# Kernel tuning notes

Measured on AMD Instinct MI355X. Metric: run time of the kernel, lower is better.

## Reference

```python
import jax, jax.numpy as jnp
import numpy as np

N_NODES = 40000


def gcn_conv(x, edge_index, W, b, num_nodes):
    """PyG GCNConv: add self-loops, sym-normalize, x @ W.T then scatter-add, + bias."""
    src = edge_index[0]
    dst = edge_index[1]
    loop = jnp.arange(num_nodes, dtype=src.dtype)
    src = jnp.concatenate([src, loop])
    dst = jnp.concatenate([dst, loop])
    # linear transform first (PyG applies lin before propagate)
    h = x @ W.T  # [N, out]
    # symmetric normalization: deg over destination (with self-loops)
    deg = jax.ops.segment_sum(jnp.ones_like(dst, dtype=h.dtype), dst, num_segments=num_nodes)
    dinv = jnp.where(deg > 0, jax.lax.rsqrt(deg), 0.0)
    norm = dinv[src] * dinv[dst]  # [E+N]
    msg = h[src] * norm[:, None]  # gather + scale
    out = jax.ops.segment_sum(msg, dst, num_segments=num_nodes)  # scatter-add
    return out + b


def setup_inputs() -> dict:
    key = jax.random.key(0)
    k1, k2, k3, k4, k5, k6, k7 = jax.random.split(key, 7)
    C, H, F_out = 128, 128, 1
    E = 640000
    x = jax.random.normal(k1, (N_NODES, C), dtype=jnp.float32)
    edge_index = jax.random.randint(k2, (2, E), 0, N_NODES, dtype=jnp.int64)
    # Glorot-ish init for conv weights (PyG lin.weight shape [out, in]), zero bias
    W1 = jax.random.normal(k3, (H, C), dtype=jnp.float32) / np.sqrt(C)
    b1 = jnp.zeros((H,), dtype=jnp.float32)
    W2 = jax.random.normal(k4, (F_out, H), dtype=jnp.float32) / np.sqrt(H)
    b2 = jnp.zeros((F_out,), dtype=jnp.float32)
    return {"x": x, "edge_index": edge_index, "W1": W1, "b1": b1, "W2": W2, "b2": b2}


def reference(x, edge_index, W1, b1, W2, b2):
    h = gcn_conv(x, edge_index, W1, b1, N_NODES)
    h = jax.nn.relu(h)
    out = gcn_conv(h, edge_index, W2, b2, N_NODES)
    return jax.nn.sigmoid(out)
```

## Files before the change

### kernel.cpp

```cpp
#include <hip/hip_runtime.h>
#include <math.h>
#include <stdint.h>

#define FDIM 128
#define CAP 64

typedef __bf16 bf16x8 __attribute__((ext_vector_type(8)));
typedef float f32x4 __attribute__((ext_vector_type(4)));

__device__ __forceinline__ ushort f2bf(float f) {
    uint32_t u = __float_as_uint(f);
    uint32_t r = (u >> 16) & 1;
    return (ushort)((u + 0x7fffu + r) >> 16);
}


#define XS 136

__global__ __launch_bounds__(256) void k_linear1_mfma(const float* __restrict__ x,
                                                      const float* __restrict__ W,
                                                      int* __restrict__ cnt,
                                                      ushort* __restrict__ h, int n) {
    __shared__ __align__(16) ushort Wl[128 * XS];
    __shared__ __align__(16) ushort Xl[64 * XS];

    int tid = threadIdx.x;

    if (tid < 128) {
        int g = blockIdx.x * 128 + tid;
        if (g < n) cnt[g] = 0;
    }

#pragma unroll
    for (int i = 0; i < 16; ++i) {
        int q = tid + i * 256;
        int j = q >> 5;
        int c0 = (q & 31) * 4;
        float4 v = *(const float4*)(W + (size_t)q * 4);
        uint2 p;
        p.x = (uint32_t)f2bf(v.x) | ((uint32_t)f2bf(v.y) << 16);
        p.y = (uint32_t)f2bf(v.z) | ((uint32_t)f2bf(v.w) << 16);
        *(uint2*)&Wl[j * XS + c0] = p;
    }

    int lane = tid & 63, wid = tid >> 6;
    int m0 = (wid >> 1) * 32;
    int j0 = (wid & 1) * 64;
    int lrow = lane & 15, kg = lane >> 4;

    for (int t = 0; t < 2; ++t) {
        int node0 = blockIdx.x * 128 + t * 64;
        if (node0 >= n) break;

        __syncthreads();
#pragma unroll
        for (int i = 0; i < 8; ++i) {
            int q = tid + i * 256;
            int r = q >> 5;
            int c0 = (q & 31) * 4;
            int gr = node0 + r;
            float4 v = make_float4(0.f, 0.f, 0.f, 0.f);
            if (gr < n) v = *(const float4*)(x + (size_t)gr * FDIM + c0);
            uint2 p;
            p.x = (uint32_t)f2bf(v.x) | ((uint32_t)f2bf(v.y) << 16);
            p.y = (uint32_t)f2bf(v.z) | ((uint32_t)f2bf(v.w) << 16);
            *(uint2*)&Xl[r * XS + c0] = p;
        }
        __syncthreads();

        bf16x8 af[2][4];
#pragma unroll
        for (int mt = 0; mt < 2; ++mt)
#pragma unroll
            for (int ks = 0; ks < 4; ++ks)
                af[mt][ks] = *(const bf16x8*)&Xl[(m0 + mt * 16 + lrow) * XS + ks * 32 + kg * 8];

        f32x4 acc[2][4] = {};
#pragma unroll
        for (int jt = 0; jt < 4; ++jt) {
            bf16x8 bfr[4];
#pragma unroll
            for (int ks = 0; ks < 4; ++ks)
                bfr[ks] = *(const bf16x8*)&Wl[(j0 + jt * 16 + lrow) * XS + ks * 32 + kg * 8];
#pragma unroll
            for (int mt = 0; mt < 2; ++mt)
#pragma unroll
                for (int ks = 0; ks < 4; ++ks)
                    acc[mt][jt] = __builtin_amdgcn_mfma_f32_16x16x32_bf16(
                        af[mt][ks], bfr[ks], acc[mt][jt], 0, 0, 0);
        }

#pragma unroll
        for (int mt = 0; mt < 2; ++mt)
#pragma unroll
            for (int jt = 0; jt < 4; ++jt)
#pragma unroll
                for (int r = 0; r < 4; ++r) {
                    int gi = node0 + m0 + mt * 16 + kg * 4 + r;
                    int gj = j0 + jt * 16 + lrow;
                    if (gi < n) h[(size_t)gi * FDIM + gj] = f2bf(acc[mt][jt][r]);
                }
    }
}


__global__ __launch_bounds__(256) void k_scatter_ell(const int* __restrict__ src,
                                                     const int* __restrict__ dst,
                                                     int* __restrict__ cnt,
                                                     ushort* __restrict__ ell, int E) {
    int e = blockIdx.x * blockDim.x + threadIdx.x;
    if (e < E) {
        int d = dst[e];
        int p = atomicAdd(&cnt[d], 1);
        if (p < CAP) ell[(size_t)d * CAP + p] = (ushort)src[e];
    }
}


__device__ __forceinline__ float bf_lo(uint32_t u) { return __uint_as_float(u << 16); }
__device__ __forceinline__ float bf_hi(uint32_t u) { return __uint_as_float(u & 0xFFFF0000u); }

__global__ __launch_bounds__(256) void k_agg1_h2(const uint32_t* __restrict__ h,
                                                 const ushort* __restrict__ ell,
                                                 const int* __restrict__ cnt,
                                                 const float* __restrict__ b1,
                                                 const float* __restrict__ W2,
                                                 float* __restrict__ h2s, int n) {
    int gtid = blockIdx.x * blockDim.x + threadIdx.x;
    int d = gtid >> 6;
    int lane = threadIdx.x & 63;
    if (d >= n) return;

    int degt = cnt[d];
    int deg = min(degt, CAP);
    int myidx = 0;
    float mydv = 0.f;
    if (lane < deg) {
        myidx = (int)ell[(size_t)d * CAP + lane];
        mydv = rsqrtf((float)cnt[myidx] + 1.0f);
    }

    float dd = rsqrtf((float)degt + 1.0f);
    uint32_t u = h[(size_t)d * 64 + lane];
    float ax[8], ay[8];
    ax[0] = bf_lo(u) * dd; ay[0] = bf_hi(u) * dd;
#pragma unroll
    for (int r = 1; r < 8; ++r) { ax[r] = 0.f; ay[r] = 0.f; }

    int k = 0;
    for (; k + 7 < deg; k += 8) {
        int s[8]; float dv[8]; uint32_t uu[8];
#pragma unroll
        for (int r = 0; r < 8; ++r) { s[r] = __shfl(myidx, k + r); dv[r] = __shfl(mydv, k + r); }
#pragma unroll
        for (int r = 0; r < 8; ++r) uu[r] = h[(size_t)s[r] * 64 + lane];
#pragma unroll
        for (int r = 0; r < 8; ++r) { ax[r] += bf_lo(uu[r]) * dv[r]; ay[r] += bf_hi(uu[r]) * dv[r]; }
    }
    for (; k + 3 < deg; k += 4) {
        int s[4]; float dv[4]; uint32_t uu[4];
#pragma unroll
        for (int r = 0; r < 4; ++r) { s[r] = __shfl(myidx, k + r); dv[r] = __shfl(mydv, k + r); }
#pragma unroll
        for (int r = 0; r < 4; ++r) uu[r] = h[(size_t)s[r] * 64 + lane];
#pragma unroll
        for (int r = 0; r < 4; ++r) { ax[r] += bf_lo(uu[r]) * dv[r]; ay[r] += bf_hi(uu[r]) * dv[r]; }
    }
    for (; k < deg; ++k) {
        int s0 = __shfl(myidx, k);
        float dv0 = __shfl(mydv, k);
        uint32_t u0 = h[(size_t)s0 * 64 + lane];
        ax[0] += bf_lo(u0) * dv0; ay[0] += bf_hi(u0) * dv0;
    }

    float sx = ((ax[0] + ax[1]) + (ax[2] + ax[3])) + ((ax[4] + ax[5]) + (ax[6] + ax[7]));
    float sy = ((ay[0] + ay[1]) + (ay[2] + ay[3])) + ((ay[4] + ay[5]) + (ay[6] + ay[7]));

    float ox = sx * dd;
    float oy = sy * dd;

    float2 bb = *(const float2*)(b1 + lane * 2);
    float2 ww = *(const float2*)(W2 + lane * 2);
    float s = fmaxf(ox + bb.x, 0.f) * ww.x + fmaxf(oy + bb.y, 0.f) * ww.y;
#pragma unroll
    for (int o = 32; o; o >>= 1) s += __shfl_down(s, o);
    if (lane == 0) h2s[d] = s * dd;
}


__global__ __launch_bounds__(256) void k_agg2(const float* __restrict__ h2s,
                                              const ushort* __restrict__ ell,
                                              const int* __restrict__ cnt,
                                              const float* __restrict__ b2,
                                              float* __restrict__ out, int n) {
    int gtid = blockIdx.x * blockDim.x + threadIdx.x;
    int i = gtid >> 6;
    int lane = threadIdx.x & 63;
    if (i >= n) return;

    int degt = cnt[i];
    int deg = min(degt, CAP);
    float v = 0.f;
    if (lane < deg) {
        int s = ell[(size_t)i * CAP + lane];
        v = h2s[s];
    }
#pragma unroll
    for (int o = 32; o; o >>= 1) v += __shfl_down(v, o);
    if (lane == 0) {
        float dd = rsqrtf((float)degt + 1.0f);
        float r = (h2s[i] + v) * dd + b2[0];
        out[i] = 1.f / (1.f + expf(-r));
    }
}


extern "C" void kernel_launch(void* const* d_in, const int* in_sizes, int n_in,
                              void* d_out, int out_size, void* d_ws, size_t ws_size,
                              hipStream_t stream) {
    const float* x  = (const float*)d_in[0];
    const int*   ei = (const int*)d_in[1];
    const float* W1 = (const float*)d_in[2];
    const float* b1 = (const float*)d_in[3];
    const float* W2 = (const float*)d_in[4];
    const float* b2 = (const float*)d_in[5];

    int n = out_size;
    int E = in_sizes[1] / 2;
    const int* src = ei;
    const int* dst = ei + E;

    char* w = (char*)d_ws;
    int*    cnt = (int*)w;     w += (size_t)((n + 3) & ~3) * 4;
    ushort* ell = (ushort*)w;  w += (size_t)n * CAP * 2;
    ushort* h1s = (ushort*)w;  w += (size_t)n * FDIM * 2;
    float*  h2s = (float*)w;   w += (size_t)n * 4;

    int nblk_lin = (n + 127) / 128;

    k_linear1_mfma<<<nblk_lin, 256, 0, stream>>>(x, W1, cnt, h1s, n);
    k_scatter_ell<<<(E + 255) / 256, 256, 0, stream>>>(src, dst, cnt, ell, E);
    k_agg1_h2<<<(n * 64 + 255) / 256, 256, 0, stream>>>((const uint32_t*)h1s, ell, cnt, b1, W2, h2s, n);
    k_agg2<<<(n * 64 + 255) / 256, 256, 0, stream>>>(h2s, ell, cnt, b2, (float*)d_out, n);
}
```

Baseline: 85.58 us.

## Merge linear and edge-scatter kernels, pre-convert W1 to bf16 in prep kernel

Adds a small prep kernel that converts W1 to padded bf16 once and zeroes the degree counters with int4 stores. The linear MFMA kernel and the ELL scatter kernel become one launch, with block ranges split by role, so the atomic scatter can overlap the GEMM. Each linear block now covers 256 nodes instead of 128, which amortises the W tile copy into LDS. The scatter blocks still allocate the large LDS footprint, which may limit how many run at once, and an extra launch is added.

```diff
diff --git a/kernel.cpp b/kernel.cpp
--- a/kernel.cpp
+++ b/kernel.cpp
@@ -4,6 +4,7 @@
 
 #define FDIM 128
 #define CAP 64
+#define XS 136
 
 typedef __bf16 bf16x8 __attribute__((ext_vector_type(8)));
 typedef float f32x4 __attribute__((ext_vector_type(4)));
@@ -15,32 +16,52 @@
 }
 
 
-#define XS 136
-
-__global__ __launch_bounds__(256) void k_linear1_mfma(const float* __restrict__ x,
-                                                      const float* __restrict__ W,
-                                                      int* __restrict__ cnt,
-                                                      ushort* __restrict__ h, int n) {
-    __shared__ __align__(16) ushort Wl[128 * XS];
-    __shared__ __align__(16) ushort Xl[64 * XS];
-
-    int tid = threadIdx.x;
-
-    if (tid < 128) {
-        int g = blockIdx.x * 128 + tid;
-        if (g < n) cnt[g] = 0;
-    }
-
-#pragma unroll
-    for (int i = 0; i < 16; ++i) {
-        int q = tid + i * 256;
-        int j = q >> 5;
-        int c0 = (q & 31) * 4;
-        float4 v = *(const float4*)(W + (size_t)q * 4);
+__global__ __launch_bounds__(256) void k_prep(const float* __restrict__ W,
+                                              ushort* __restrict__ Wb,
+                                              int4* __restrict__ cnt4, int n4) {
+    int t = blockIdx.x * blockDim.x + threadIdx.x;
+    if (t < 4096) {
+        float4 v = *(const float4*)(W + (size_t)t * 4);
+        int j = t >> 5, c0 = (t & 31) * 4;
         uint2 p;
         p.x = (uint32_t)f2bf(v.x) | ((uint32_t)f2bf(v.y) << 16);
         p.y = (uint32_t)f2bf(v.z) | ((uint32_t)f2bf(v.w) << 16);
-        *(uint2*)&Wl[j * XS + c0] = p;
+        *(uint2*)&Wb[j * XS + c0] = p;
+    } else {
+        int z = t - 4096;
+        if (z < n4) cnt4[z] = make_int4(0, 0, 0, 0);
+    }
+}
+
+
+__global__ __launch_bounds__(256) void k_lin_scatter(const float* __restrict__ x,
+                                                     const ushort* __restrict__ Wb,
+                                                     const int* __restrict__ src,
+                                                     const int* __restrict__ dst,
+                                                     int* __restrict__ cnt,
+                                                     ushort* __restrict__ ell,
+                                                     ushort* __restrict__ h,
+                                                     int n, int E) {
+    int NL = (n + 255) >> 8;
+    int tid = threadIdx.x;
+
+    if ((int)blockIdx.x >= NL) {
+        int e = ((int)blockIdx.x - NL) * 256 + tid;
+        if (e < E) {
+            int d = dst[e];
+            int p = atomicAdd(&cnt[d], 1);
+            if (p < CAP) ell[(size_t)d * CAP + p] = (ushort)src[e];
+        }
+        return;
+    }
+
+    __shared__ __align__(16) ushort Wl[128 * XS];
+    __shared__ __align__(16) ushort Xl[64 * XS];
+
+    {
+        const uint4* wsrc = (const uint4*)Wb;
+        uint4* wdst = (uint4*)Wl;
+        for (int i = tid; i < (128 * XS) / 8; i += 256) wdst[i] = wsrc[i];
     }
 
     int lane = tid & 63, wid = tid >> 6;
@@ -48,8 +69,8 @@
     int j0 = (wid & 1) * 64;
     int lrow = lane & 15, kg = lane >> 4;
 
-    for (int t = 0; t < 2; ++t) {
-        int node0 = blockIdx.x * 128 + t * 64;
+    for (int t = 0; t < 4; ++t) {
+        int node0 = (int)blockIdx.x * 256 + t * 64;
         if (node0 >= n) break;
 
         __syncthreads();
@@ -104,19 +125,6 @@
 }
 
 
-__global__ __launch_bounds__(256) void k_scatter_ell(const int* __restrict__ src,
-                                                     const int* __restrict__ dst,
-                                                     int* __restrict__ cnt,
-                                                     ushort* __restrict__ ell, int E) {
-    int e = blockIdx.x * blockDim.x + threadIdx.x;
-    if (e < E) {
-        int d = dst[e];
-        int p = atomicAdd(&cnt[d], 1);
-        if (p < CAP) ell[(size_t)d * CAP + p] = (ushort)src[e];
-    }
-}
-
-
 __device__ __forceinline__ float bf_lo(uint32_t u) { return __uint_as_float(u << 16); }
 __device__ __forceinline__ float bf_hi(uint32_t u) { return __uint_as_float(u & 0xFFFF0000u); }
 
@@ -232,14 +240,18 @@
 
     char* w = (char*)d_ws;
     int*    cnt = (int*)w;     w += (size_t)((n + 3) & ~3) * 4;
+    ushort* Wb  = (ushort*)w;  w += (size_t)128 * XS * 2;
     ushort* ell = (ushort*)w;  w += (size_t)n * CAP * 2;
     ushort* h1s = (ushort*)w;  w += (size_t)n * FDIM * 2;
     float*  h2s = (float*)w;   w += (size_t)n * 4;
 
-    int nblk_lin = (n + 127) / 128;
-
-    k_linear1_mfma<<<nblk_lin, 256, 0, stream>>>(x, W1, cnt, h1s, n);
-    k_scatter_ell<<<(E + 255) / 256, 256, 0, stream>>>(src, dst, cnt, ell, E);
+    int n4 = ((n + 3) & ~3) / 4;
+    int nblk_prep = (4096 + n4 + 255) / 256;
+    int NL = (n + 255) / 256;
+    int nblk_merged = NL + (E + 255) / 256;
+
+    k_prep<<<nblk_prep, 256, 0, stream>>>(W1, Wb, (int4*)cnt, n4);
+    k_lin_scatter<<<nblk_merged, 256, 0, stream>>>(x, Wb, src, dst, cnt, ell, h1s, n, E);
     k_agg1_h2<<<(n * 64 + 255) / 256, 256, 0, stream>>>((const uint32_t*)h1s, ell, cnt, b1, W2, h2s, n);
     k_agg2<<<(n * 64 + 255) / 256, 256, 0, stream>>>(h2s, ell, cnt, b2, (float*)d_out, n);
 }
```

After: 94.68 us. +10.6%, slower.
